# Kernel tuning notes

Measured on AMD Instinct MI355X. Metric: run time of the kernel, lower is better.

## Reference

```python
import jax, jax.numpy as jnp
import numpy as np
from jax import lax

K = 3        # kernel_size
PAD = 1      # padding
STRIDE = 1   # stride


def conv2d(x, w, stride, pad):
    return lax.conv_general_dilated(
        x, w, (stride, stride), [(pad, pad), (pad, pad)],
        dimension_numbers=('NCHW', 'OIHW', 'NCHW'))


def setup_inputs() -> dict:
    key = jax.random.key(0)
    ks = jax.random.split(key, 8)
    B, Ci, Cc, H, W = 8, 64, 64, 128, 128
    K2 = K * K
    return {
        'x_img': jax.random.normal(ks[0], (B, Ci, H, W), jnp.float32),
        'x_cont': jax.random.normal(ks[1], (B, Cc, H, W), jnp.float32),
        'w_fuse': jax.random.normal(ks[2], (Ci, Ci + Cc, 1, 1), jnp.float32) * 0.05,
        'w_off': jax.random.normal(ks[3], (2 * K2, Ci, K, K), jnp.float32) * 0.01,
        'b_off': jax.random.normal(ks[4], (2 * K2,), jnp.float32) * 0.1,
        'w_mod': jax.random.normal(ks[5], (K2, Ci, K, K), jnp.float32) * 0.01,
        'b_mod': jax.random.normal(ks[6], (K2,), jnp.float32) * 0.1,
        'w_reg': jax.random.normal(ks[7], (Ci, Ci, K, K), jnp.float32) * 0.05,
    }


def _bilinear_sample(img, py, px):
    # Zero padding outside the image (per-corner validity, matches torchvision).
    C, Hin, Win = img.shape
    flat = img.reshape(C, -1)
    y0 = jnp.floor(py)
    x0 = jnp.floor(px)

    def gather(yy, xx):
        valid = (yy >= 0) & (yy <= Hin - 1) & (xx >= 0) & (xx <= Win - 1)
        yc = jnp.clip(yy, 0, Hin - 1).astype(jnp.int32)
        xc = jnp.clip(xx, 0, Win - 1).astype(jnp.int32)
        return flat[:, yc * Win + xc] * valid[None].astype(img.dtype)

    wy1 = py - y0; wy0 = 1.0 - wy1
    wx1 = px - x0; wx0 = 1.0 - wx1
    return (gather(y0, x0) * (wy0 * wx0)[None]
            + gather(y0, x0 + 1.0) * (wy0 * wx1)[None]
            + gather(y0 + 1.0, x0) * (wy1 * wx0)[None]
            + gather(y0 + 1.0, x0 + 1.0) * (wy1 * wx1)[None])


def reference(x_img, x_cont, w_fuse, w_off, b_off, w_mod, b_mod, w_reg):
    # 1x1 fuse of image features with control factor
    x = conv2d(jnp.concatenate([x_img, x_cont], axis=1), w_fuse, 1, 0)
    # offset / modulator branches
    off = conv2d(x, w_off, STRIDE, PAD) + b_off[None, :, None, None]
    mod = 2.0 * jax.nn.sigmoid(conv2d(x, w_mod, STRIDE, PAD) + b_mod[None, :, None, None])
    B, C, Hin, Win = x.shape
    K2 = K * K
    Hout, Wout = off.shape[2], off.shape[3]
    # torchvision layout: channel 2k = dy, 2k+1 = dx for kernel pos k = i*K + j
    off = off.reshape(B, K2, 2, Hout, Wout)
    dy, dx = off[:, :, 0], off[:, :, 1]
    ky = (jnp.arange(K2) // K).astype(x.dtype)
    kx = (jnp.arange(K2) % K).astype(x.dtype)
    base_y = (jnp.arange(Hout) * STRIDE - PAD).astype(x.dtype)
    base_x = (jnp.arange(Wout) * STRIDE - PAD).astype(x.dtype)
    py = dy + base_y[None, None, :, None] + ky[None, :, None, None]  # [B,K2,H,W]
    px = dx + base_x[None, None, None, :] + kx[None, :, None, None]
    sampled = jax.vmap(_bilinear_sample)(x, py, px)          # [B,C,K2,H,W]
    sampled = sampled * mod[:, None]                          # modulation
    out = jnp.einsum('oik,bikhw->bohw', w_reg.reshape(C, C, K2), sampled)
    return out
```

## Files before the change

### kernel.cpp

```cpp
#include <hip/hip_runtime.h>
#include <math.h>

#define B_   8
#define C_   64
#define H_   128
#define W_   128
#define HW_  16384
#define K2_  9

typedef float f32x4 __attribute__((ext_vector_type(4)));
typedef short bf16x8 __attribute__((ext_vector_type(8)));
typedef unsigned short u16x4 __attribute__((ext_vector_type(4)));
typedef unsigned int u32x4 __attribute__((ext_vector_type(4)));

#define WS_WRP  8192
#define WS_WRP2 26624
#define WS_XT   45056
#define WS_OM   8433664

static __device__ __forceinline__ unsigned short f2bf(float x) {
    unsigned int u = __float_as_uint(x);
    unsigned int r = (u + 0x7fffu + ((u >> 16) & 1u)) >> 16;
    return (unsigned short)r;
}
static __device__ __forceinline__ float bf2f(unsigned short u) {
    return __uint_as_float(((unsigned int)u) << 16);
}
static __device__ __forceinline__ unsigned int cvt_pk_bf16(float lo, float hi) {
    unsigned int r;
    asm("v_cvt_pk_bf16_f32 %0, %1, %2" : "=v"(r) : "v"(lo), "v"(hi));
    return r;
}
static __device__ __forceinline__ u32x4 sel4(bool c, u32x4 a, u32x4 b) {
    u32x4 r;
    r[0] = c ? a[0] : b[0];
    r[1] = c ? a[1] : b[1];
    r[2] = c ? a[2] : b[2];
    r[3] = c ? a[3] : b[3];
    return r;
}

__global__ __launch_bounds__(256) void k_fuse(const float* __restrict__ xi,
                                              const float* __restrict__ xc,
                                              const float* __restrict__ wf,
                                              const float* __restrict__ wreg,
                                              const float* __restrict__ wOff,
                                              const float* __restrict__ wMod,
                                              unsigned short* __restrict__ xtb,
                                              unsigned short* __restrict__ wrP,
                                              unsigned short* __restrict__ wrP2) {
    __shared__ unsigned short sA[1024 * 8];
    const int t = threadIdx.x;
    const int lane = t & 63;
    const int wv = t >> 6;
    const int b = blockIdx.x & 7;
    const int yh = blockIdx.x >> 3;
    const int y = yh >> 1;
    const int h = yh & 1;

    if (blockIdx.x < 18) {
        const int idx = blockIdx.x * 256 + t;
        if (idx < 4608) {
            int ln = idx & 63, mt = (idx >> 6) & 3, kc = (idx >> 8) & 1, tap = idx >> 9;
            int o = mt * 16 + (ln & 15);
            int ibase = kc * 32 + (ln >> 4) * 8;
#pragma unroll
            for (int j = 0; j < 8; ++j)
                wrP[idx * 8 + j] = f2bf(wreg[(o * 64 + ibase + j) * 9 + tap]);
        }
        if (idx < 2304) {
            int ln = idx & 63, mt = (idx >> 6) & 1, kc = idx >> 7;
            int m = mt * 16 + (ln & 15);
            int gkb = kc * 32 + (ln >> 4) * 8;
#pragma unroll
            for (int j = 0; j < 8; ++j) {
                int gk = gkb + j, tap = gk >> 6, ci = gk & 63;
                float v = 0.f;
                if (m < 18)      v = wOff[(m * 64 + ci) * 9 + tap];
                else if (m < 27) v = wMod[((m - 18) * 64 + ci) * 9 + tap];
                wrP2[idx * 8 + j] = f2bf(v);
            }
        }
    }

#pragma unroll
    for (int r = 0; r < 4; ++r) {
        const int c = t + 256 * r;
        const int f = c >> 6;
        const int ln = c & 63;
        const int mt = f & 3, kc = f >> 2;
        const int m = mt * 16 + (ln & 15);
        const int kb = kc * 32 + (ln >> 4) * 8;
        const float* s = wf + m * 128 + kb;
        unsigned short us[8];
#pragma unroll
        for (int j = 0; j < 8; ++j) us[j] = f2bf(s[j]);
        *(bf16x8*)&sA[c * 8] = *(const bf16x8*)us;
    }
    __syncthreads();

    const int n15 = lane & 15;
    const int q4 = lane >> 4;
    const int px = h * 64 + wv * 16 + n15;
    const size_t poff = (size_t)y * W_ + px;

    f32x4 acc[4];
#pragma unroll
    for (int mt = 0; mt < 4; ++mt) acc[mt] = (f32x4){0.f, 0.f, 0.f, 0.f};

#pragma unroll
    for (int kc = 0; kc < 4; ++kc) {
        const float* src = (kc < 2)
            ? (xi + ((size_t)(b * 64 + kc * 32 + q4 * 8)) * HW_ + poff)
            : (xc + ((size_t)(b * 64 + (kc - 2) * 32 + q4 * 8)) * HW_ + poff);
        unsigned short us[8];
#pragma unroll
        for (int j = 0; j < 8; ++j) us[j] = f2bf(src[(size_t)j * HW_]);
        const bf16x8 bf = *(const bf16x8*)us;
#pragma unroll
        for (int mt = 0; mt < 4; ++mt) {
            const bf16x8 a = *(const bf16x8*)&sA[((kc * 4 + mt) * 64 + lane) * 8];
            acc[mt] = __builtin_amdgcn_mfma_f32_16x16x32_bf16(a, bf, acc[mt], 0, 0, 0);
        }
    }

#pragma unroll
    for (int mt = 0; mt < 4; ++mt) {
        u16x4 o4;
        o4.x = f2bf(acc[mt][0]); o4.y = f2bf(acc[mt][1]);
        o4.z = f2bf(acc[mt][2]); o4.w = f2bf(acc[mt][3]);
        *(u16x4*)&xtb[((size_t)b * HW_ + poff) * 64 + mt * 16 + q4 * 4] = o4;
    }
}

__global__ __launch_bounds__(256) void k_offmod(const unsigned short* __restrict__ xtb,
                                                const unsigned short* __restrict__ wrP2,
                                                const float* __restrict__ bOff,
                                                const float* __restrict__ bMod,
                                                float* __restrict__ om) {
    __shared__ unsigned short sB[3 * 66 * 72];
    const int t = threadIdx.x;
    const int lane = t & 63;
    const int wv = t >> 6;
    const int b = blockIdx.x & 7;
    const int yh = blockIdx.x >> 3;
    const int y = yh >> 1;
    const int h = yh & 1;

    for (int idx = t; idx < 3 * 66 * 8; idx += 256) {
        const int c8 = idx & 7;
        const int pp = (idx >> 3) % 66;
        const int row = (idx >> 3) / 66;
        const int gx = h * 64 + pp - 1;
        const int gy = y + row - 1;
        bf16x8 v = {0, 0, 0, 0, 0, 0, 0, 0};
        if (gx >= 0 && gx < W_ && gy >= 0 && gy < H_)
            v = *(const bf16x8*)&xtb[(((size_t)(b * H_ + gy)) * W_ + gx) * 64 + c8 * 8];
        *(bf16x8*)&sB[(row * 66 + pp) * 72 + c8 * 8] = v;
    }
    __syncthreads();

    const int n15 = lane & 15;
    const int q4 = lane >> 4;

    f32x4 acc[2];
    acc[0] = (f32x4){0.f, 0.f, 0.f, 0.f};
    acc[1] = (f32x4){0.f, 0.f, 0.f, 0.f};

#pragma unroll
    for (int kc = 0; kc < 18; ++kc) {
        const int gkb = kc * 32 + q4 * 8;
        const int tap = gkb >> 6;
        const int ci = gkb & 63;
        const int row = tap / 3, kx = tap % 3;
        const bf16x8 bf = *(const bf16x8*)&sB[(row * 66 + (wv * 16 + n15 + kx)) * 72 + ci];
        const bf16x8 a0 = *(const bf16x8*)(wrP2 + (((size_t)(kc * 2 + 0) * 64 + lane) * 8));
        const bf16x8 a1 = *(const bf16x8*)(wrP2 + (((size_t)(kc * 2 + 1) * 64 + lane) * 8));
        acc[0] = __builtin_amdgcn_mfma_f32_16x16x32_bf16(a0, bf, acc[0], 0, 0, 0);
        acc[1] = __builtin_amdgcn_mfma_f32_16x16x32_bf16(a1, bf, acc[1], 0, 0, 0);
    }

    const int px = h * 64 + wv * 16 + n15;
    const size_t rec = ((size_t)(b * H_ + y)) * 28 * 128;
#pragma unroll
    for (int mt = 0; mt < 2; ++mt)
#pragma unroll
        for (int r = 0; r < 4; ++r) {
            const int o = mt * 16 + q4 * 4 + r;
            if (o < 18) {
                const int c = (o >> 1) + ((o & 1) ? 9 : 0);
                om[rec + c * 128 + px] = acc[mt][r] + bOff[o];
            } else if (o < 27) {
                const float z = acc[mt][r] + bMod[o - 18];
                om[rec + (18 + (o - 18)) * 128 + px] = 2.f / (1.f + __expf(-z));
            }
        }
}

__global__ __launch_bounds__(256) void k_deform(const unsigned short* __restrict__ xtb,
                                                const float* __restrict__ om,
                                                const unsigned short* __restrict__ wrP,
                                                float* __restrict__ out) {
    __shared__ __align__(16) unsigned short sW[5 * 68 * 72];
    const int t = threadIdx.x;
    const int lane = t & 63;
    const int wv = t >> 6;
    const int b = blockIdx.x & 7;
    const int yh = blockIdx.x >> 3;
    const int y = yh >> 1;
    const int h = yh & 1;
    const int wx0 = h * 64 - 2;
    const int ylo = y - 2;

    for (int i = t; i < 2720; i += 256) {
        const int c8 = i & 7;
        const int p  = (i >> 3) % 68;
        const int r  = (i >> 3) / 68;
        const int gx = wx0 + p;
        const int gy = ylo + r;
        bf16x8 v = {0, 0, 0, 0, 0, 0, 0, 0};
        if (gx >= 0 && gx < W_ && gy >= 0 && gy < H_)
            v = *(const bf16x8*)&xtb[(((size_t)(b * H_ + gy)) * W_ + gx) * 64 + c8 * 8];
        *(bf16x8*)&sW[(r * 68 + p) * 72 + c8 * 8] = v;
    }
    __syncthreads();

    const char* xbB = (const char*)(xtb + (size_t)b * HW_ * 64);
    const float* omr = om + ((size_t)(b * H_ + y)) * 28 * 128;

    const int n15 = lane & 15;
    const int q4 = lane >> 4;
    const int px = h * 64 + wv * 16 + n15;

    float omv[27];
#pragma unroll
    for (int i = 0; i < 27; ++i) omv[i] = omr[i * 128 + px];

    f32x4 acc[4];
#pragma unroll
    for (int mt = 0; mt < 4; ++mt) acc[mt] = (f32x4){0.f, 0.f, 0.f, 0.f};

    for (int k = 0; k < 9; ++k) {
        const int ky = k / 3 - 1, kx = k % 3 - 1;
        const float dy  = omv[k];
        const float dxv = omv[9 + k];
        const float m   = omv[18 + k];
        const float py  = (float)(y + ky) + dy;
        const float pxe = (float)(px + kx) + dxv;
        const float y0f = floorf(py), x0f = floorf(pxe);
        const int y0i = (int)y0f, x0i = (int)x0f;
        const float wy1 = py - y0f, wx1 = pxe - x0f;
        const float wy0 = 1.f - wy1, wx0f = 1.f - wx1;

        u32x4 gv[8];
        float wts[4];
#pragma unroll
        for (int c = 0; c < 4; ++c) {
            const int cy = c >> 1, cx = c & 1;
            const int yy = y0i + cy;
            const int xx = x0i + cx;
            const bool ok = (yy >= 0) && (yy < H_) && (xx >= 0) && (xx < W_);
            wts[c] = ok ? (cy ? wy1 : wy0) * (cx ? wx1 : wx0f) * m : 0.f;
            const bool inw = (yy >= ylo) && (yy <= ylo + 4)
                          && (xx >= wx0) && (xx < wx0 + 68);
            int wr = yy - ylo; wr = min(max(wr, 0), 4);
            int wc = xx - wx0; wc = min(max(wc, 0), 67);
            const int lsW = (wr * 68 + wc) * 72 + q4 * 8;
            const bf16x8 l0 = *(const bf16x8*)&sW[lsW];
            const bf16x8 l1 = *(const bf16x8*)&sW[lsW + 32];
            const int yc = min(max(yy, 0), H_ - 1);
            const int xc = min(max(xx, 0), W_ - 1);
            const int off = inw ? (q4 * 16) : ((yc * W_ + xc) * 128 + q4 * 16);
            const bf16x8 g0 = *(const bf16x8*)(xbB + off);
            const bf16x8 g1 = *(const bf16x8*)(xbB + off + 64);
            u32x4 lu0, lu1, gu0, gu1;
            __builtin_memcpy(&lu0, &l0, 16);
            __builtin_memcpy(&lu1, &l1, 16);
            __builtin_memcpy(&gu0, &g0, 16);
            __builtin_memcpy(&gu1, &g1, 16);
            gv[c]     = sel4(inw, lu0, gu0);
            gv[4 + c] = sel4(inw, lu1, gu1);
        }

        const float w0 = wts[0], w1 = wts[1], w2 = wts[2], w3 = wts[3];
#pragma unroll
        for (int kc = 0; kc < 2; ++kc) {
            unsigned int outw[4];
#pragma unroll
            for (int d = 0; d < 4; ++d) {
                const unsigned int av = gv[kc * 4 + 0][d];
                const unsigned int bv = gv[kc * 4 + 1][d];
                const unsigned int cv = gv[kc * 4 + 2][d];
                const unsigned int ev = gv[kc * 4 + 3][d];
                const float lo = __uint_as_float(av << 16) * w0
                               + __uint_as_float(bv << 16) * w1
                               + __uint_as_float(cv << 16) * w2
                               + __uint_as_float(ev << 16) * w3;
                const float hi = __uint_as_float(av & 0xffff0000u) * w0
                               + __uint_as_float(bv & 0xffff0000u) * w1
                               + __uint_as_float(cv & 0xffff0000u) * w2
                               + __uint_as_float(ev & 0xffff0000u) * w3;
                outw[d] = cvt_pk_bf16(lo, hi);
            }
            const bf16x8 bfB = *(const bf16x8*)outw;
#pragma unroll
            for (int mt = 0; mt < 4; ++mt) {
                const bf16x8 a = *(const bf16x8*)(wrP +
                    ((((size_t)((k * 2 + kc) * 4 + mt)) * 64 + lane) * 8));
                acc[mt] = __builtin_amdgcn_mfma_f32_16x16x32_bf16(a, bfB, acc[mt], 0, 0, 0);
            }
        }
    }

#pragma unroll
    for (int mt = 0; mt < 4; ++mt)
#pragma unroll
        for (int r = 0; r < 4; ++r) {
            const int o = mt * 16 + q4 * 4 + r;
            out[(((size_t)(b * 64 + o)) * H_ + y) * W_ + px] = acc[mt][r];
        }
}

extern "C" void kernel_launch(void* const* d_in, const int* in_sizes, int n_in,
                              void* d_out, int out_size, void* d_ws, size_t ws_size,
                              hipStream_t stream) {
    const float* x_img  = (const float*)d_in[0];
    const float* x_cont = (const float*)d_in[1];
    const float* w_fuse = (const float*)d_in[2];
    const float* w_off  = (const float*)d_in[3];
    const float* b_off  = (const float*)d_in[4];
    const float* w_mod  = (const float*)d_in[5];
    const float* b_mod  = (const float*)d_in[6];
    const float* w_reg  = (const float*)d_in[7];
    float* out = (float*)d_out;

    float* ws  = (float*)d_ws;
    unsigned short* wrP  = (unsigned short*)(ws + WS_WRP);
    unsigned short* wrP2 = (unsigned short*)(ws + WS_WRP2);
    unsigned short* xtb  = (unsigned short*)(ws + WS_XT);
    float* om  = ws + WS_OM;

    k_fuse<<<B_ * H_ * 2, 256, 0, stream>>>(x_img, x_cont, w_fuse, w_reg, w_off,
                                            w_mod, xtb, wrP, wrP2);
    k_offmod<<<B_ * H_ * 2, 256, 0, stream>>>(xtb, wrP2, b_off, b_mod, om);
    k_deform<<<B_ * H_ * 2, 256, 0, stream>>>(xtb, om, wrP, out);
}
```

Before: 194.5 us.

## Fuse offset/modulator conv into deformable sampling kernel via shared memory

Merges the offset/modulator 3x3 conv kernel into the deformable-sampling kernel. The conv now reads its input from the 5-row halo tile already staged in LDS and passes its results through a small shared array instead of global memory. This removes one kernel launch, the om buffer write and read round trip, and a second staging of the x tile. In exchange the fused kernel does more work per block, uses more LDS, and adds an extra barrier, which may reduce occupancy.

```diff
diff --git a/kernel.cpp b/kernel.cpp
--- a/kernel.cpp
+++ b/kernel.cpp
@@ -16,7 +16,6 @@
 #define WS_WRP  8192
 #define WS_WRP2 26624
 #define WS_XT   45056
-#define WS_OM   8433664
 
 static __device__ __forceinline__ unsigned short f2bf(float x) {
     unsigned int u = __float_as_uint(x);
@@ -133,75 +132,14 @@
     }
 }
 
-__global__ __launch_bounds__(256) void k_offmod(const unsigned short* __restrict__ xtb,
-                                                const unsigned short* __restrict__ wrP2,
-                                                const float* __restrict__ bOff,
-                                                const float* __restrict__ bMod,
-                                                float* __restrict__ om) {
-    __shared__ unsigned short sB[3 * 66 * 72];
-    const int t = threadIdx.x;
-    const int lane = t & 63;
-    const int wv = t >> 6;
-    const int b = blockIdx.x & 7;
-    const int yh = blockIdx.x >> 3;
-    const int y = yh >> 1;
-    const int h = yh & 1;
-
-    for (int idx = t; idx < 3 * 66 * 8; idx += 256) {
-        const int c8 = idx & 7;
-        const int pp = (idx >> 3) % 66;
-        const int row = (idx >> 3) / 66;
-        const int gx = h * 64 + pp - 1;
-        const int gy = y + row - 1;
-        bf16x8 v = {0, 0, 0, 0, 0, 0, 0, 0};
-        if (gx >= 0 && gx < W_ && gy >= 0 && gy < H_)
-            v = *(const bf16x8*)&xtb[(((size_t)(b * H_ + gy)) * W_ + gx) * 64 + c8 * 8];
-        *(bf16x8*)&sB[(row * 66 + pp) * 72 + c8 * 8] = v;
-    }
-    __syncthreads();
-
-    const int n15 = lane & 15;
-    const int q4 = lane >> 4;
-
-    f32x4 acc[2];
-    acc[0] = (f32x4){0.f, 0.f, 0.f, 0.f};
-    acc[1] = (f32x4){0.f, 0.f, 0.f, 0.f};
-
-#pragma unroll
-    for (int kc = 0; kc < 18; ++kc) {
-        const int gkb = kc * 32 + q4 * 8;
-        const int tap = gkb >> 6;
-        const int ci = gkb & 63;
-        const int row = tap / 3, kx = tap % 3;
-        const bf16x8 bf = *(const bf16x8*)&sB[(row * 66 + (wv * 16 + n15 + kx)) * 72 + ci];
-        const bf16x8 a0 = *(const bf16x8*)(wrP2 + (((size_t)(kc * 2 + 0) * 64 + lane) * 8));
-        const bf16x8 a1 = *(const bf16x8*)(wrP2 + (((size_t)(kc * 2 + 1) * 64 + lane) * 8));
-        acc[0] = __builtin_amdgcn_mfma_f32_16x16x32_bf16(a0, bf, acc[0], 0, 0, 0);
-        acc[1] = __builtin_amdgcn_mfma_f32_16x16x32_bf16(a1, bf, acc[1], 0, 0, 0);
-    }
-
-    const int px = h * 64 + wv * 16 + n15;
-    const size_t rec = ((size_t)(b * H_ + y)) * 28 * 128;
-#pragma unroll
-    for (int mt = 0; mt < 2; ++mt)
-#pragma unroll
-        for (int r = 0; r < 4; ++r) {
-            const int o = mt * 16 + q4 * 4 + r;
-            if (o < 18) {
-                const int c = (o >> 1) + ((o & 1) ? 9 : 0);
-                om[rec + c * 128 + px] = acc[mt][r] + bOff[o];
-            } else if (o < 27) {
-                const float z = acc[mt][r] + bMod[o - 18];
-                om[rec + (18 + (o - 18)) * 128 + px] = 2.f / (1.f + __expf(-z));
-            }
-        }
-}
-
-__global__ __launch_bounds__(256) void k_deform(const unsigned short* __restrict__ xtb,
-                                                const float* __restrict__ om,
-                                                const unsigned short* __restrict__ wrP,
-                                                float* __restrict__ out) {
+__global__ __launch_bounds__(256) void k_od(const unsigned short* __restrict__ xtb,
+                                            const unsigned short* __restrict__ wrP2,
+                                            const unsigned short* __restrict__ wrP,
+                                            const float* __restrict__ bOff,
+                                            const float* __restrict__ bMod,
+                                            float* __restrict__ out) {
     __shared__ __align__(16) unsigned short sW[5 * 68 * 72];
+    __shared__ float omS[4][27][16];
     const int t = threadIdx.x;
     const int lane = t & 63;
     const int wv = t >> 6;
@@ -225,16 +163,48 @@
     }
     __syncthreads();
 
-    const char* xbB = (const char*)(xtb + (size_t)b * HW_ * 64);
-    const float* omr = om + ((size_t)(b * H_ + y)) * 28 * 128;
-
     const int n15 = lane & 15;
     const int q4 = lane >> 4;
     const int px = h * 64 + wv * 16 + n15;
 
+    {
+        f32x4 accO[2];
+        accO[0] = (f32x4){0.f, 0.f, 0.f, 0.f};
+        accO[1] = (f32x4){0.f, 0.f, 0.f, 0.f};
+#pragma unroll
+        for (int kc = 0; kc < 18; ++kc) {
+            const int gkb = kc * 32 + q4 * 8;
+            const int tap = gkb >> 6;
+            const int ci = gkb & 63;
+            const int row = tap / 3, kx = tap % 3;
+            const bf16x8 bf = *(const bf16x8*)
+                &sW[((row + 1) * 68 + (wv * 16 + n15 + kx + 1)) * 72 + ci];
+            const bf16x8 a0 = *(const bf16x8*)(wrP2 + (((size_t)(kc * 2 + 0) * 64 + lane) * 8));
+            const bf16x8 a1 = *(const bf16x8*)(wrP2 + (((size_t)(kc * 2 + 1) * 64 + lane) * 8));
+            accO[0] = __builtin_amdgcn_mfma_f32_16x16x32_bf16(a0, bf, accO[0], 0, 0, 0);
+            accO[1] = __builtin_amdgcn_mfma_f32_16x16x32_bf16(a1, bf, accO[1], 0, 0, 0);
+        }
+#pragma unroll
+        for (int mt = 0; mt < 2; ++mt)
+#pragma unroll
+            for (int r = 0; r < 4; ++r) {
+                const int o = mt * 16 + q4 * 4 + r;
+                if (o < 18) {
+                    const int c = (o >> 1) + ((o & 1) ? 9 : 0);
+                    omS[wv][c][n15] = accO[mt][r] + bOff[o];
+                } else if (o < 27) {
+                    const float z = accO[mt][r] + bMod[o - 18];
+                    omS[wv][o][n15] = 2.f / (1.f + __expf(-z));
+                }
+            }
+    }
+    __syncthreads();
+
+    const char* xbB = (const char*)(xtb + (size_t)b * HW_ * 64);
+
     float omv[27];
 #pragma unroll
-    for (int i = 0; i < 27; ++i) omv[i] = omr[i * 128 + px];
+    for (int i = 0; i < 27; ++i) omv[i] = omS[wv][i][n15];
 
     f32x4 acc[4];
 #pragma unroll
@@ -338,10 +308,8 @@
     unsigned short* wrP  = (unsigned short*)(ws + WS_WRP);
     unsigned short* wrP2 = (unsigned short*)(ws + WS_WRP2);
     unsigned short* xtb  = (unsigned short*)(ws + WS_XT);
-    float* om  = ws + WS_OM;
 
     k_fuse<<<B_ * H_ * 2, 256, 0, stream>>>(x_img, x_cont, w_fuse, w_reg, w_off,
                                             w_mod, xtb, wrP, wrP2);
-    k_offmod<<<B_ * H_ * 2, 256, 0, stream>>>(xtb, wrP2, b_off, b_mod, om);
-    k_deform<<<B_ * H_ * 2, 256, 0, stream>>>(xtb, om, wrP, out);
-}
+    k_od<<<B_ * H_ * 2, 256, 0, stream>>>(xtb, wrP2, wrP, b_off, b_mod, out);
+}
```

Result: no change. 197.6 us (+1.5%).
